# Kernel tuning notes

Hardware: AMD Instinct MI355X
Metric: run time of the kernel (lower is better)

Reference implementation:

```python
import jax, jax.numpy as jnp
import numpy as np

B, T, C, H = 4, 2048, 1024, 16
D = C // H  # head dim = 64

def setup_inputs() -> dict:
    key = jax.random.key(0)
    ks = jax.random.split(key, 5)
    s = 0.02
    return {
        "x": jax.random.normal(ks[0], (B, T, C), dtype=jnp.float32),
        # torch Linear convention: weight shape (out, in), y = x @ W.T + b
        "Wqkv": jax.random.normal(ks[1], (3 * C, C), dtype=jnp.float32) * s,
        "bqkv": jax.random.normal(ks[2], (3 * C,), dtype=jnp.float32) * s,
        "Wproj": jax.random.normal(ks[3], (C, C), dtype=jnp.float32) * s,
        "bproj": jax.random.normal(ks[4], (C,), dtype=jnp.float32) * s,
    }

def reference(x, Wqkv, bqkv, Wproj, bproj):
    b, t, c = x.shape
    qkv = x @ Wqkv.T + bqkv                      # [B,T,3C]
    q, k, v = jnp.split(qkv, 3, axis=-1)
    # [B,T,C] -> [B,H,T,D]
    q = q.reshape(b, t, H, D).transpose(0, 2, 1, 3)
    k = k.reshape(b, t, H, D).transpose(0, 2, 1, 3)
    v = v.reshape(b, t, H, D).transpose(0, 2, 1, 3)
    scale = 1.0 / jnp.sqrt(jnp.float32(D))
    att = jnp.einsum('bhqd,bhkd->bhqk', q, k) * scale   # [B,H,T,T]
    # additive causal mask: -inf strictly above diagonal
    mask = jnp.triu(jnp.full((t, t), -jnp.inf, dtype=att.dtype), k=1)
    att = att + mask
    att = jax.nn.softmax(att, axis=-1)
    # dropout p=0.0 -> identity
    y = jnp.einsum('bhqk,bhkd->bhqd', att, v)            # [B,H,T,D]
    y = y.transpose(0, 2, 1, 3).reshape(b, t, c)         # [B,T,C]
    y = y @ Wproj.T + bproj
    return y
```

## Files before the change

### kernel.cpp

```cpp
#include <hip/hip_runtime.h>
#include <hip/hip_bf16.h>
#include <stdint.h>

constexpr int BB = 4, TT = 2048, CC = 1024, HH = 16, DD = 64;

typedef __bf16 bf16_t;
typedef bf16_t bf16x8 __attribute__((ext_vector_type(8)));
typedef float f32x4 __attribute__((ext_vector_type(4)));

__device__ __forceinline__ unsigned short f2bf(float f) {
    union { __bf16 h; unsigned short u; } v;
    v.h = (__bf16)f;
    return v.u;
}

__device__ __forceinline__ f32x4 mfma16(bf16x8 a, bf16x8 b, f32x4 c) {
    return __builtin_amdgcn_mfma_f32_16x16x32_bf16(a, b, c, 0, 0, 0);
}

#define LOAD_LDS16(g, l)                                                      \
    __builtin_amdgcn_global_load_lds(                                         \
        (const __attribute__((address_space(1))) void*)(g),                   \
        (__attribute__((address_space(3))) void*)(l), 16, 0, 0)

__global__ __launch_bounds__(256) void cvt_all(
    const float* __restrict__ a, long na,
    const float* __restrict__ b, long nb,
    const float* __restrict__ c, long nc,
    unsigned short* __restrict__ oa, unsigned short* __restrict__ ob,
    unsigned short* __restrict__ oc) {
    const long ntot = na + nb + nc;
    long i = (long)blockIdx.x * blockDim.x + threadIdx.x;
    const long stride = (long)gridDim.x * blockDim.x;
    for (; i < ntot; i += stride) {
        const float* src;
        unsigned short* dst;
        long q = i;
        if (q < na) { src = a; dst = oa; }
        else if (q < na + nb) { q -= na; src = b; dst = ob; }
        else { q -= na + nb; src = c; dst = oc; }
        float4 v = *(const float4*)(src + q * 4);
        ushort4 o;
        o.x = f2bf(v.x); o.y = f2bf(v.y); o.z = f2bf(v.z); o.w = f2bf(v.w);
        *(ushort4*)(dst + q * 4) = o;
    }
}

template <int MODE>
__global__ __launch_bounds__(256, 3) void gemm_bt(
    const unsigned short* __restrict__ A,
    const unsigned short* __restrict__ Bw,
    const float* __restrict__ bias,
    unsigned short* __restrict__ qb, unsigned short* __restrict__ kb,
    unsigned short* __restrict__ vtb, float* __restrict__ outf,
    int M, int N, int K) {
    __shared__ __align__(16) unsigned short smem[17408];
    unsigned short* Asb = smem;
    unsigned short* Bsb = smem + 8192;
    const int tid = threadIdx.x;
    const int w = tid >> 6, lane = tid & 63;
    const int g = lane >> 4, q16 = lane & 15;
    const int wr = w >> 1, wc = w & 1;
    const int mbase = blockIdx.x * 128;
    const int nbase = blockIdx.y * 128;
    const int srow = lane >> 2;
    const int scol = (lane & 3) * 8;

    f32x4 acc[4][4];
#pragma unroll
    for (int i = 0; i < 4; ++i)
#pragma unroll
        for (int j = 0; j < 4; ++j) acc[i][j] = (f32x4){0.f, 0.f, 0.f, 0.f};

    const int nk = K >> 5;

    auto stage = [&](int buf, int t) {
        const int k0 = t << 5;
#pragma unroll
        for (int ii = 0; ii < 2; ++ii) {
            const int i = w + ii * 4;
            const unsigned short* ga =
                A + (long)(mbase + i * 16 + srow) * K + k0 + scol;
            LOAD_LDS16(ga, &Asb[buf * 4096 + i * 512]);
            const unsigned short* gb =
                Bw + (long)(nbase + i * 16 + srow) * K + k0 + scol;
            LOAD_LDS16(gb, &Bsb[buf * 4096 + i * 512]);
        }
    };

    stage(0, 0);
    __syncthreads();
    int cur = 0;
    for (int t = 0; t < nk; ++t) {
        if (t + 1 < nk) stage(cur ^ 1, t + 1);
        bf16x8 af[4], bfr[4];
#pragma unroll
        for (int mi = 0; mi < 4; ++mi)
            af[mi] = *(const bf16x8*)&Asb[cur * 4096 +
                                          (wr * 64 + mi * 16 + q16) * 32 + 8 * g];
#pragma unroll
        for (int ni = 0; ni < 4; ++ni)
            bfr[ni] = *(const bf16x8*)&Bsb[cur * 4096 +
                                           (wc * 64 + ni * 16 + q16) * 32 + 8 * g];
#pragma unroll
        for (int mi = 0; mi < 4; ++mi)
#pragma unroll
            for (int ni = 0; ni < 4; ++ni)
                acc[mi][ni] = mfma16(af[mi], bfr[ni], acc[mi][ni]);
        __syncthreads();
        cur ^= 1;
    }

    if (MODE == 0 && (nbase >> 10) == 2) {
        const int bb = mbase >> 11, t0 = mbase & 2047;
        const int h0 = (nbase & 1023) >> 6;
#pragma unroll
        for (int mi = 0; mi < 4; ++mi) {
#pragma unroll
            for (int ni = 0; ni < 4; ++ni) {
                const int nl = wc * 64 + ni * 16 + q16;
                const int hh = nl >> 6, d = nl & 63;
                const float bv = bias[nbase + nl];
                ushort4 pk;
                pk.x = f2bf(acc[mi][ni][0] + bv);
                pk.y = f2bf(acc[mi][ni][1] + bv);
                pk.z = f2bf(acc[mi][ni][2] + bv);
                pk.w = f2bf(acc[mi][ni][3] + bv);
                const int tb = wr * 64 + mi * 16 + 4 * g;
                const int cp = (tb >> 3) ^ (d & 7);
                const int pos = cp * 8 + (tb & 7);
                *(ushort4*)&smem[hh * 8704 + d * 136 + pos] = pk;
            }
        }
        __syncthreads();
#pragma unroll
        for (int it = 0; it < 8; ++it) {
            const int task = it * 256 + tid;
            const int hh = task >> 10, d = (task >> 4) & 63, cr = task & 15;
            const int cp = cr ^ (d & 7);
            uint4 v4 = *(const uint4*)&smem[hh * 8704 + d * 136 + cp * 8];
            const long off =
                ((long)(bb * HH + h0 + hh) * DD + d) * TT + t0 + cr * 8;
            *(uint4*)&vtb[off] = v4;
        }
        return;
    }

#pragma unroll
    for (int mi = 0; mi < 4; ++mi) {
#pragma unroll
        for (int ni = 0; ni < 4; ++ni) {
            const int n = nbase + wc * 64 + ni * 16 + q16;
            const float bv = bias[n];
#pragma unroll
            for (int r = 0; r < 4; ++r) {
                const int m = mbase + wr * 64 + mi * 16 + 4 * g + r;
                const float val = acc[mi][ni][r] + bv;
                if (MODE == 0) {
                    const int which = n >> 10, rem = n & 1023;
                    const int h = rem >> 6, d = rem & 63;
                    const int b = m >> 11, t = m & 2047;
                    const long bh = (long)(b * HH + h);
                    if (which == 0)
                        qb[(bh * TT + t) * DD + d] =
                            f2bf(val * 0.18033688011112042f);
                    else
                        kb[(bh * TT + t) * DD + d] = f2bf(val);
                } else {
                    outf[(long)m * N + n] = val;
                }
            }
        }
    }
}

__global__ __launch_bounds__(256, 4) void attn_fwd(
    const unsigned short* __restrict__ qb, const unsigned short* __restrict__ kb,
    const unsigned short* __restrict__ vtb, unsigned short* __restrict__ attb) {
    __shared__ __align__(16) unsigned short Ks[2][64 * 64];
    __shared__ __align__(16) unsigned short Vs[2][64 * 64];
    __shared__ __align__(16) unsigned short plds[4][16 * 64];
    const int tid = threadIdx.x;
    const int w = tid >> 6, lane = tid & 63;
    const int g = lane >> 4, q16 = lane & 15;
    const int bid = blockIdx.x;
    const int swz = (bid & 7) * 256 + (bid >> 3);
    const int bx = 31 - (swz & 31);
    const int bh = swz >> 5;
    const int b = bh >> 4, h = bh & 15;
    const int qbase = bx * 64 + w * 16;

    const unsigned short* Q = qb + (long)bh * TT * DD;
    const unsigned short* Kp = kb + (long)bh * TT * DD;
    const unsigned short* Vt = vtb + (long)bh * DD * TT;

    const int srow = tid >> 3;
    const int ssl = ((tid & 7) ^ (srow & 7)) * 8;
    unsigned short* kdst0 = &Ks[0][0] + w * 512;
    unsigned short* vdst0 = &Vs[0][0] + w * 512;

    auto stageKV = [&](int buf, int kt) {
        const long kb0 = (long)kt * 64;
        const unsigned short* gk = Kp + (kb0 + srow) * DD + ssl;
        const unsigned short* gv = Vt + (long)srow * TT + kb0 + ssl;
        unsigned short* kd = kdst0 + buf * 4096;
        unsigned short* vd = vdst0 + buf * 4096;
        LOAD_LDS16(gk, kd);
        LOAD_LDS16(gk + 32l * DD, kd + 2048);
        LOAD_LDS16(gv, vd);
        LOAD_LDS16(gv + 32l * TT, vd + 2048);
    };

    bf16x8 aq0 = *(const bf16x8*)&Q[(qbase + q16) * DD + 8 * g];
    bf16x8 aq1 = *(const bf16x8*)&Q[(qbase + q16) * DD + 32 + 8 * g];

    f32x4 acc[4];
#pragma unroll
    for (int i = 0; i < 4; ++i) acc[i] = (f32x4){0.f, 0.f, 0.f, 0.f};
    float mrow = -1e30f, lrow = 0.f;

    const int slot0 = (g ^ (q16 & 7)) << 3;
    const int nkt = bx + 1;
    stageKV(0, 0);
    __syncthreads();
    int cur = 0;
    for (int kt = 0; kt < nkt; ++kt) {
        if (kt + 1 < nkt) stageKV(cur ^ 1, kt + 1);
        const int kbase = kt * 64;
        f32x4 p[4];
#pragma unroll
        for (int s = 0; s < 4; ++s) p[s] = (f32x4){0.f, 0.f, 0.f, 0.f};
        __builtin_amdgcn_s_setprio(1);
#pragma unroll
        for (int s = 0; s < 4; ++s) {
            const int kr = (16 * s + q16) * 64;
            bf16x8 bk0 = *(const bf16x8*)&Ks[cur][kr + slot0];
            bf16x8 bk1 = *(const bf16x8*)&Ks[cur][kr + (slot0 ^ 32)];
            p[s] = mfma16(bk0, aq0, p[s]);
            p[s] = mfma16(bk1, aq1, p[s]);
        }
        __builtin_amdgcn_s_setprio(0);
        const int q = qbase + q16;
        if (kt == nkt - 1) {
#pragma unroll
            for (int s = 0; s < 4; ++s)
#pragma unroll
                for (int r = 0; r < 4; ++r)
                    if (kbase + 16 * s + 4 * g + r > q) p[s][r] = -1e30f;
        }
        float t = fmaxf(fmaxf(p[0][0], p[0][1]), fmaxf(p[0][2], p[0][3]));
#pragma unroll
        for (int s = 1; s < 4; ++s)
            t = fmaxf(t, fmaxf(fmaxf(p[s][0], p[s][1]), fmaxf(p[s][2], p[s][3])));
        if (__all(t - mrow <= 11.541560327111708f)) {
            float ssum = 0.f;
#pragma unroll
            for (int s = 0; s < 4; ++s)
#pragma unroll
                for (int r = 0; r < 4; ++r) {
                    p[s][r] = __builtin_amdgcn_exp2f(p[s][r] - mrow);
                    ssum += p[s][r];
                }
            lrow += ssum;
        } else {
            t = fmaxf(t, __shfl_xor(t, 16));
            t = fmaxf(t, __shfl_xor(t, 32));
            const float nm = fmaxf(mrow, t);
            const float fs = __builtin_amdgcn_exp2f(mrow - nm);
            mrow = nm;
            float ssum = 0.f;
#pragma unroll
            for (int s = 0; s < 4; ++s)
#pragma unroll
                for (int r = 0; r < 4; ++r) {
                    p[s][r] = __builtin_amdgcn_exp2f(p[s][r] - nm);
                    ssum += p[s][r];
                }
            lrow = lrow * fs + ssum;
            float fr[4];
#pragma unroll
            for (int r = 0; r < 4; ++r) fr[r] = __shfl(fs, 4 * g + r);
#pragma unroll
            for (int ni = 0; ni < 4; ++ni)
#pragma unroll
                for (int r = 0; r < 4; ++r) acc[ni][r] *= fr[r];
        }
#pragma unroll
        for (int s = 0; s < 4; ++s) {
            ushort4 pk;
            pk.x = f2bf(p[s][0]); pk.y = f2bf(p[s][1]);
            pk.z = f2bf(p[s][2]); pk.w = f2bf(p[s][3]);
            const int Gp = ((2 * s + (g >> 1)) ^ (q16 & 7)) * 8 + (g & 1) * 4;
            *(ushort4*)&plds[w][q16 * 64 + Gp] = pk;
        }
        bf16x8 pa0 = *(const bf16x8*)&plds[w][q16 * 64 + slot0];
        bf16x8 pa1 = *(const bf16x8*)&plds[w][q16 * 64 + (slot0 ^ 32)];
        __builtin_amdgcn_s_setprio(1);
#pragma unroll
        for (int ni = 0; ni < 4; ++ni) {
            const int vr = (ni * 16 + q16) * 64;
            bf16x8 bv0 = *(const bf16x8*)&Vs[cur][vr + slot0];
            bf16x8 bv1 = *(const bf16x8*)&Vs[cur][vr + (slot0 ^ 32)];
            acc[ni] = mfma16(pa0, bv0, acc[ni]);
            acc[ni] = mfma16(pa1, bv1, acc[ni]);
        }
        __builtin_amdgcn_s_setprio(0);
        __syncthreads();
        cur ^= 1;
    }
    lrow += __shfl_xor(lrow, 16);
    lrow += __shfl_xor(lrow, 32);
    float inv[4];
#pragma unroll
    for (int r = 0; r < 4; ++r) inv[r] = 1.0f / __shfl(lrow, 4 * g + r);
#pragma unroll
    for (int ni = 0; ni < 4; ++ni)
#pragma unroll
        for (int r = 0; r < 4; ++r) {
            const int q = qbase + 4 * g + r;
            const int d = ni * 16 + q16;
            attb[(((long)b * TT + q) * HH + h) * DD + d] =
                f2bf(acc[ni][r] * inv[r]);
        }
}

extern "C" void kernel_launch(void* const* d_in, const int* in_sizes, int n_in,
                              void* d_out, int out_size, void* d_ws, size_t ws_size,
                              hipStream_t stream) {
    const float* x = (const float*)d_in[0];
    const float* Wqkv = (const float*)d_in[1];
    const float* bqkv = (const float*)d_in[2];
    const float* Wproj = (const float*)d_in[3];
    const float* bproj = (const float*)d_in[4];
    float* out = (float*)d_out;

    char* ws = (char*)d_ws;
    unsigned short* xb = (unsigned short*)(ws);
    unsigned short* wqkvb = (unsigned short*)(ws + (16l << 20));
    unsigned short* wprojb = (unsigned short*)(ws + (22l << 20));
    unsigned short* qb = (unsigned short*)(ws + (24l << 20));
    unsigned short* kb = (unsigned short*)(ws + (40l << 20));
    unsigned short* vtb = (unsigned short*)(ws + (56l << 20));
    unsigned short* attb = xb;

    cvt_all<<<2048, 256, 0, stream>>>(
        x, (long)BB * TT * CC / 4, Wqkv, (long)3 * CC * CC / 4, Wproj,
        (long)CC * CC / 4, xb, wqkvb, wprojb);

    gemm_bt<0><<<dim3(64, 24), 256, 0, stream>>>(xb, wqkvb, bqkv, qb, kb, vtb,
                                                 nullptr, BB * TT, 3 * CC, CC);
    attn_fwd<<<2048, 256, 0, stream>>>(qb, kb, vtb, attb);
    gemm_bt<1><<<dim3(64, 8), 256, 0, stream>>>(attb, wprojb, bproj, nullptr,
                                                nullptr, nullptr, out, BB * TT,
                                                CC, CC);
}
```

Measured before the change: 183.4 us.

## Process two query sub-tiles per attention block to reuse staged K/V tiles

Each attention block now handles 128 query rows as two 64-row sub-tiles sharing the same staged K and V tiles in LDS, halving the grid. This is meant to halve K/V global loads and LDS staging per query and amortise synchronisation. In exchange it raises register pressure (two accumulator sets), which is why the occupancy hint drops from 4 to 3 blocks. Load balancing across blocks also gets coarser.

```diff
diff --git a/kernel.cpp b/kernel.cpp
--- a/kernel.cpp
+++ b/kernel.cpp
@@ -157,11 +157,11 @@
                 const int m = mbase + wr * 64 + mi * 16 + 4 * g + r;
                 const float val = acc[mi][ni][r] + bv;
                 if (MODE == 0) {
-                    const int which = n >> 10, rem = n & 1023;
+                    const int rem = n & 1023;
                     const int h = rem >> 6, d = rem & 63;
                     const int b = m >> 11, t = m & 2047;
                     const long bh = (long)(b * HH + h);
-                    if (which == 0)
+                    if ((n >> 10) == 0)
                         qb[(bh * TT + t) * DD + d] =
                             f2bf(val * 0.18033688011112042f);
                     else
@@ -174,7 +174,7 @@
     }
 }
 
-__global__ __launch_bounds__(256, 4) void attn_fwd(
+__global__ __launch_bounds__(256, 3) void attn_fwd(
     const unsigned short* __restrict__ qb, const unsigned short* __restrict__ kb,
     const unsigned short* __restrict__ vtb, unsigned short* __restrict__ attb) {
     __shared__ __align__(16) unsigned short Ks[2][64 * 64];
@@ -184,11 +184,12 @@
     const int w = tid >> 6, lane = tid & 63;
     const int g = lane >> 4, q16 = lane & 15;
     const int bid = blockIdx.x;
-    const int swz = (bid & 7) * 256 + (bid >> 3);
-    const int bx = 31 - (swz & 31);
-    const int bh = swz >> 5;
+    const int swz = (bid & 7) * 128 + (bid >> 3);
+    const int bxp = 15 - (swz & 15);
+    const int bh = swz >> 4;
     const int b = bh >> 4, h = bh & 15;
-    const int qbase = bx * 64 + w * 16;
+    const int qs0 = bxp * 128 + w * 16;
+    const int qs1 = qs0 + 64;
 
     const unsigned short* Q = qb + (long)bh * TT * DD;
     const unsigned short* Kp = kb + (long)bh * TT * DD;
@@ -211,117 +212,146 @@
         LOAD_LDS16(gv + 32l * TT, vd + 2048);
     };
 
-    bf16x8 aq0 = *(const bf16x8*)&Q[(qbase + q16) * DD + 8 * g];
-    bf16x8 aq1 = *(const bf16x8*)&Q[(qbase + q16) * DD + 32 + 8 * g];
-
-    f32x4 acc[4];
-#pragma unroll
-    for (int i = 0; i < 4; ++i) acc[i] = (f32x4){0.f, 0.f, 0.f, 0.f};
-    float mrow = -1e30f, lrow = 0.f;
+    bf16x8 aq[2][2];
+    aq[0][0] = *(const bf16x8*)&Q[(qs0 + q16) * DD + 8 * g];
+    aq[0][1] = *(const bf16x8*)&Q[(qs0 + q16) * DD + 32 + 8 * g];
+    aq[1][0] = *(const bf16x8*)&Q[(qs1 + q16) * DD + 8 * g];
+    aq[1][1] = *(const bf16x8*)&Q[(qs1 + q16) * DD + 32 + 8 * g];
+
+    f32x4 acc[2][4];
+#pragma unroll
+    for (int js = 0; js < 2; ++js)
+#pragma unroll
+        for (int i = 0; i < 4; ++i) acc[js][i] = (f32x4){0.f, 0.f, 0.f, 0.f};
+    float mrow[2] = {-1e30f, -1e30f}, lrow[2] = {0.f, 0.f};
 
     const int slot0 = (g ^ (q16 & 7)) << 3;
-    const int nkt = bx + 1;
+    const int nkt = 2 * bxp + 2;
     stageKV(0, 0);
     __syncthreads();
     int cur = 0;
     for (int kt = 0; kt < nkt; ++kt) {
         if (kt + 1 < nkt) stageKV(cur ^ 1, kt + 1);
         const int kbase = kt * 64;
-        f32x4 p[4];
-#pragma unroll
-        for (int s = 0; s < 4; ++s) p[s] = (f32x4){0.f, 0.f, 0.f, 0.f};
-        __builtin_amdgcn_s_setprio(1);
+        const bool live0 = (kt <= 2 * bxp);
+        bf16x8 pa[2][2];
+
+        bf16x8 bk[4][2];
 #pragma unroll
         for (int s = 0; s < 4; ++s) {
             const int kr = (16 * s + q16) * 64;
-            bf16x8 bk0 = *(const bf16x8*)&Ks[cur][kr + slot0];
-            bf16x8 bk1 = *(const bf16x8*)&Ks[cur][kr + (slot0 ^ 32)];
-            p[s] = mfma16(bk0, aq0, p[s]);
-            p[s] = mfma16(bk1, aq1, p[s]);
-        }
-        __builtin_amdgcn_s_setprio(0);
-        const int q = qbase + q16;
-        if (kt == nkt - 1) {
-#pragma unroll
-            for (int s = 0; s < 4; ++s)
-#pragma unroll
-                for (int r = 0; r < 4; ++r)
-                    if (kbase + 16 * s + 4 * g + r > q) p[s][r] = -1e30f;
-        }
-        float t = fmaxf(fmaxf(p[0][0], p[0][1]), fmaxf(p[0][2], p[0][3]));
-#pragma unroll
-        for (int s = 1; s < 4; ++s)
-            t = fmaxf(t, fmaxf(fmaxf(p[s][0], p[s][1]), fmaxf(p[s][2], p[s][3])));
-        if (__all(t - mrow <= 11.541560327111708f)) {
-            float ssum = 0.f;
-#pragma unroll
-            for (int s = 0; s < 4; ++s)
-#pragma unroll
-                for (int r = 0; r < 4; ++r) {
-                    p[s][r] = __builtin_amdgcn_exp2f(p[s][r] - mrow);
-                    ssum += p[s][r];
-                }
-            lrow += ssum;
-        } else {
-            t = fmaxf(t, __shfl_xor(t, 16));
-            t = fmaxf(t, __shfl_xor(t, 32));
-            const float nm = fmaxf(mrow, t);
-            const float fs = __builtin_amdgcn_exp2f(mrow - nm);
-            mrow = nm;
-            float ssum = 0.f;
-#pragma unroll
-            for (int s = 0; s < 4; ++s)
-#pragma unroll
-                for (int r = 0; r < 4; ++r) {
-                    p[s][r] = __builtin_amdgcn_exp2f(p[s][r] - nm);
-                    ssum += p[s][r];
-                }
-            lrow = lrow * fs + ssum;
-            float fr[4];
-#pragma unroll
-            for (int r = 0; r < 4; ++r) fr[r] = __shfl(fs, 4 * g + r);
-#pragma unroll
-            for (int ni = 0; ni < 4; ++ni)
-#pragma unroll
-                for (int r = 0; r < 4; ++r) acc[ni][r] *= fr[r];
-        }
-#pragma unroll
-        for (int s = 0; s < 4; ++s) {
-            ushort4 pk;
-            pk.x = f2bf(p[s][0]); pk.y = f2bf(p[s][1]);
-            pk.z = f2bf(p[s][2]); pk.w = f2bf(p[s][3]);
-            const int Gp = ((2 * s + (g >> 1)) ^ (q16 & 7)) * 8 + (g & 1) * 4;
-            *(ushort4*)&plds[w][q16 * 64 + Gp] = pk;
-        }
-        bf16x8 pa0 = *(const bf16x8*)&plds[w][q16 * 64 + slot0];
-        bf16x8 pa1 = *(const bf16x8*)&plds[w][q16 * 64 + (slot0 ^ 32)];
+            bk[s][0] = *(const bf16x8*)&Ks[cur][kr + slot0];
+            bk[s][1] = *(const bf16x8*)&Ks[cur][kr + (slot0 ^ 32)];
+        }
+
+#pragma unroll
+        for (int js = 0; js < 2; ++js) {
+            if (js == 0 && !live0) continue;
+            f32x4 p[4];
+#pragma unroll
+            for (int s = 0; s < 4; ++s) p[s] = (f32x4){0.f, 0.f, 0.f, 0.f};
+            __builtin_amdgcn_s_setprio(1);
+#pragma unroll
+            for (int s = 0; s < 4; ++s) {
+                p[s] = mfma16(bk[s][0], aq[js][0], p[s]);
+                p[s] = mfma16(bk[s][1], aq[js][1], p[s]);
+            }
+            __builtin_amdgcn_s_setprio(0);
+            const int qrow = (js ? qs1 : qs0) + q16;
+            const int mtile = 2 * bxp + js;
+            if (kt == mtile) {
+#pragma unroll
+                for (int s = 0; s < 4; ++s)
+#pragma unroll
+                    for (int r = 0; r < 4; ++r)
+                        if (kbase + 16 * s + 4 * g + r > qrow) p[s][r] = -1e30f;
+            }
+            float t = fmaxf(fmaxf(p[0][0], p[0][1]), fmaxf(p[0][2], p[0][3]));
+#pragma unroll
+            for (int s = 1; s < 4; ++s)
+                t = fmaxf(t, fmaxf(fmaxf(p[s][0], p[s][1]),
+                                   fmaxf(p[s][2], p[s][3])));
+            if (__all(t - mrow[js] <= 11.541560327111708f)) {
+                float ssum = 0.f;
+#pragma unroll
+                for (int s = 0; s < 4; ++s)
+#pragma unroll
+                    for (int r = 0; r < 4; ++r) {
+                        p[s][r] = __builtin_amdgcn_exp2f(p[s][r] - mrow[js]);
+                        ssum += p[s][r];
+                    }
+                lrow[js] += ssum;
+            } else {
+                t = fmaxf(t, __shfl_xor(t, 16));
+                t = fmaxf(t, __shfl_xor(t, 32));
+                const float nm = fmaxf(mrow[js], t);
+                const float fs = __builtin_amdgcn_exp2f(mrow[js] - nm);
+                mrow[js] = nm;
+                float ssum = 0.f;
+#pragma unroll
+                for (int s = 0; s < 4; ++s)
+#pragma unroll
+                    for (int r = 0; r < 4; ++r) {
+                        p[s][r] = __builtin_amdgcn_exp2f(p[s][r] - nm);
+                        ssum += p[s][r];
+                    }
+                lrow[js] = lrow[js] * fs + ssum;
+                float fr[4];
+#pragma unroll
+                for (int r = 0; r < 4; ++r) fr[r] = __shfl(fs, 4 * g + r);
+#pragma unroll
+                for (int ni = 0; ni < 4; ++ni)
+#pragma unroll
+                    for (int r = 0; r < 4; ++r) acc[js][ni][r] *= fr[r];
+            }
+#pragma unroll
+            for (int s = 0; s < 4; ++s) {
+                ushort4 pk;
+                pk.x = f2bf(p[s][0]); pk.y = f2bf(p[s][1]);
+                pk.z = f2bf(p[s][2]); pk.w = f2bf(p[s][3]);
+                const int Gp = ((2 * s + (g >> 1)) ^ (q16 & 7)) * 8 + (g & 1) * 4;
+                *(ushort4*)&plds[w][q16 * 64 + Gp] = pk;
+            }
+            pa[js][0] = *(const bf16x8*)&plds[w][q16 * 64 + slot0];
+            pa[js][1] = *(const bf16x8*)&plds[w][q16 * 64 + (slot0 ^ 32)];
+        }
+
         __builtin_amdgcn_s_setprio(1);
 #pragma unroll
         for (int ni = 0; ni < 4; ++ni) {
             const int vr = (ni * 16 + q16) * 64;
             bf16x8 bv0 = *(const bf16x8*)&Vs[cur][vr + slot0];
             bf16x8 bv1 = *(const bf16x8*)&Vs[cur][vr + (slot0 ^ 32)];
-            acc[ni] = mfma16(pa0, bv0, acc[ni]);
-            acc[ni] = mfma16(pa1, bv1, acc[ni]);
+            if (live0) {
+                acc[0][ni] = mfma16(pa[0][0], bv0, acc[0][ni]);
+                acc[0][ni] = mfma16(pa[0][1], bv1, acc[0][ni]);
+            }
+            acc[1][ni] = mfma16(pa[1][0], bv0, acc[1][ni]);
+            acc[1][ni] = mfma16(pa[1][1], bv1, acc[1][ni]);
         }
         __builtin_amdgcn_s_setprio(0);
         __syncthreads();
         cur ^= 1;
     }
-    lrow += __shfl_xor(lrow, 16);
-    lrow += __shfl_xor(lrow, 32);
-    float inv[4];
-#pragma unroll
-    for (int r = 0; r < 4; ++r) inv[r] = 1.0f / __shfl(lrow, 4 * g + r);
-#pragma unroll
-    for (int ni = 0; ni < 4; ++ni)
-#pragma unroll
-        for (int r = 0; r < 4; ++r) {
-            const int q = qbase + 4 * g + r;
-            const int d = ni * 16 + q16;
-            attb[(((long)b * TT + q) * HH + h) * DD + d] =
-                f2bf(acc[ni][r] * inv[r]);
-        }
+#pragma unroll
+    for (int js = 0; js < 2; ++js) {
+        float l = lrow[js];
+        l += __shfl_xor(l, 16);
+        l += __shfl_xor(l, 32);
+        float inv[4];
+#pragma unroll
+        for (int r = 0; r < 4; ++r) inv[r] = 1.0f / __shfl(l, 4 * g + r);
+        const int qsb = js ? qs1 : qs0;
+#pragma unroll
+        for (int ni = 0; ni < 4; ++ni)
+#pragma unroll
+            for (int r = 0; r < 4; ++r) {
+                const int q = qsb + 4 * g + r;
+                const int d = ni * 16 + q16;
+                attb[(((long)b * TT + q) * HH + h) * DD + d] =
+                    f2bf(acc[js][ni][r] * inv[r]);
+            }
+    }
 }
 
 extern "C" void kernel_launch(void* const* d_in, const int* in_sizes, int n_in,
@@ -349,7 +379,7 @@
 
     gemm_bt<0><<<dim3(64, 24), 256, 0, stream>>>(xb, wqkvb, bqkv, qb, kb, vtb,
                                                  nullptr, BB * TT, 3 * CC, CC);
-    attn_fwd<<<2048, 256, 0, stream>>>(qb, kb, vtb, attb);
+    attn_fwd<<<1024, 256, 0, stream>>>(qb, kb, vtb, attb);
     gemm_bt<1><<<dim3(64, 8), 256, 0, stream>>>(attb, wprojb, bproj, nullptr,
                                                 nullptr, nullptr, out, BB * TT,
                                                 CC, CC);
```

Result: no change. 184.7 us (+0.7%).
